# Optimization experiments

Hardware: AMD Instinct MI355X
Metric: run time of the kernel (lower is better)

## Reference

```python
import jax, jax.numpy as jnp
import numpy as np

HID, H, P, N, G, K = 2688, 64, 64, 128, 8, 4
I = H * P            # intermediate_size = 4096
GN = G * N           # groups_ssm_state_size = 1024
CONV_DIM = I + 2 * GN  # 6144
TOTAL = 2 * I + 2 * GN + H  # 10304
EPS = 1e-5


def setup_inputs() -> dict:
    key = jax.random.key(0)
    ks = jax.random.split(key, 8)
    B, T = 2, 2048
    hidden_states = jax.random.normal(ks[0], (B, T, HID), dtype=jnp.float32)
    in_proj_w = jax.random.normal(ks[1], (TOTAL, HID), dtype=jnp.float32) * 0.02
    conv_w = jax.random.normal(ks[2], (CONV_DIM, K), dtype=jnp.float32) * 0.1  # depthwise kernel
    conv_b = jnp.zeros((CONV_DIM,), dtype=jnp.float32)
    A = -jnp.exp(jax.random.normal(ks[3], (H,), dtype=jnp.float32))
    D = jnp.ones((H,), dtype=jnp.float32)
    dt_bias = jnp.ones((H,), dtype=jnp.float32)
    norm_weight = jnp.ones((I,), dtype=jnp.float32)
    out_proj_w = jax.random.normal(ks[4], (HID, I), dtype=jnp.float32) * 0.02
    return {"hidden_states": hidden_states, "in_proj_w": in_proj_w, "conv_w": conv_w,
            "conv_b": conv_b, "A": A, "D": D, "dt_bias": dt_bias,
            "norm_weight": norm_weight, "out_proj_w": out_proj_w}


def reference(hidden_states, in_proj_w, conv_w, conv_b, A, D, dt_bias, norm_weight, out_proj_w):
    B, T, _ = hidden_states.shape
    hpg = H // G  # heads per group

    # 1-2. in_proj and split
    proj = jnp.einsum('bth,oh->bto', hidden_states, in_proj_w)  # (B,T,TOTAL)
    gate = proj[..., :I]
    xBC = proj[..., I:I + CONV_DIM]
    dt = proj[..., I + CONV_DIM:]  # (B,T,H)

    # 3. causal depthwise conv1d (left-pad K-1, slice to T) + silu
    xp = jnp.pad(xBC, ((0, 0), (K - 1, 0), (0, 0)))
    conv = conv_b
    for i in range(K):  # tiny fixed kernel loop
        conv = conv + xp[:, i:i + T, :] * conv_w[:, i]
    conv = jax.nn.silu(conv)

    # 4-5. split and reshape
    x = conv[..., :I].reshape(B, T, H, P)
    Bm = conv[..., I:I + GN].reshape(B, T, G, N)
    Cm = conv[..., I + GN:].reshape(B, T, G, N)

    # 6. selective scan (precompute dt / A_bar outside the scan)
    dt_sp = jax.nn.softplus(dt + dt_bias)          # (B,T,H)
    A_bar = jnp.exp(A * dt_sp)                     # (B,T,H)
    xg = x.reshape(B, T, G, hpg, P)
    Ab = A_bar.reshape(B, T, G, hpg)
    dts = dt_sp.reshape(B, T, G, hpg)

    def step(h, inp):
        x_t, B_t, C_t, Ab_t, dt_t = inp  # (B,G,hpg,P),(B,G,N),(B,G,N),(B,G,hpg),(B,G,hpg)
        outer = dt_t[..., None, None] * x_t[..., None] * B_t[:, :, None, None, :]
        h = Ab_t[..., None, None] * h + outer      # (B,G,hpg,P,N)
        y_t = jnp.einsum('bghpn,bgn->bghp', h, C_t)
        return h, y_t

    inputs = (jnp.moveaxis(xg, 1, 0), jnp.moveaxis(Bm, 1, 0), jnp.moveaxis(Cm, 1, 0),
              jnp.moveaxis(Ab, 1, 0), jnp.moveaxis(dts, 1, 0))
    h0 = jnp.zeros((B, G, hpg, P, N), dtype=hidden_states.dtype)
    _, ys = jax.lax.scan(step, h0, inputs)         # (T,B,G,hpg,P)
    y = jnp.moveaxis(ys, 0, 1).reshape(B, T, H, P) + D[None, None, :, None] * x
    y = y.reshape(B, T, I)

    # 7. gated RMSNorm
    y = y * jax.nn.silu(gate)
    var = jnp.mean(y * y, axis=-1, keepdims=True)
    y = y * jax.lax.rsqrt(var + EPS) * norm_weight

    # 8. out_proj
    return jnp.einsum('bti,oi->bto', y, out_proj_w)
```

## Files before the change

### kernel.cpp

```cpp
#include <hip/hip_runtime.h>
#include <stdint.h>

typedef unsigned short ushort_t;
typedef __attribute__((ext_vector_type(4))) float f32x4;
typedef __attribute__((ext_vector_type(2))) float f32x2;
typedef __attribute__((ext_vector_type(8))) __bf16 bf16x8;
typedef __attribute__((ext_vector_type(4))) unsigned short u16x4;
typedef __attribute__((ext_vector_type(8))) unsigned short u16x8;

#define DEV __device__ __forceinline__

DEV void gload_lds16(const void* g, void* l) {
  __builtin_amdgcn_global_load_lds(
      (const __attribute__((address_space(1))) uint32_t*)(uintptr_t)(g),
      (__attribute__((address_space(3))) uint32_t*)(uintptr_t)(l), 16, 0, 0);
}

DEV ushort_t f2bf(float f) {
  union { float f; uint32_t u; } x; x.f = f;
  x.u += 0x7fffu + ((x.u >> 16) & 1u);
  return (ushort_t)(x.u >> 16);
}

DEV float bf2f(ushort_t u) {
  union { uint32_t u; float f; } x; x.u = (uint32_t)u << 16; return x.f;
}

DEV float siluf(float x) { return x / (1.f + expf(-x)); }

#define BAR asm volatile("s_barrier" ::: "memory")
#define LGKM0 do { asm volatile("s_waitcnt lgkmcnt(0)" ::: "memory"); \
                   __builtin_amdgcn_sched_barrier(0); } while (0)
#define VMCNT(n) asm volatile("s_waitcnt vmcnt(" #n ")" ::: "memory")

__global__ __launch_bounds__(256) void fill_kernel(float* p, float v, int n) {
  int i = blockIdx.x * 256 + threadIdx.x;
  if (i < n) p[i] = v;
}

__global__ __launch_bounds__(256) void cvt_bf16_kernel(const float* __restrict__ src,
                                                       ushort_t* __restrict__ dst,
                                                       int n_src4, int n_dst4) {
  int i = blockIdx.x * 256 + threadIdx.x;
  if (i >= n_dst4) return;
  f32x4 v;
  if (i < n_src4) v = *(const f32x4*)(src + (size_t)i * 4);
  else { v.x = 0.f; v.y = 0.f; v.z = 0.f; v.w = 0.f; }
  u16x4 o;
  o.x = f2bf(v.x); o.y = f2bf(v.y); o.z = f2bf(v.z); o.w = f2bf(v.w);
  *(u16x4*)(dst + (size_t)i * 4) = o;
}

DEV void ld_a4(const unsigned char* ab2, int mgofs, int ck0, int ck1, bf16x8 (&af)[4][2]) {
#pragma unroll
  for (int mi = 0; mi < 4; ++mi) {
    const unsigned char* p = ab2 + (mgofs + mi * 16) * 128;
    af[mi][0] = *(const bf16x8*)(p + ck0);
    af[mi][1] = *(const bf16x8*)(p + ck1);
  }
}

DEV void ld_b2(const unsigned char* bb2, int npofs, int ck0, int ck1, bf16x8 (&bf)[2][2]) {
#pragma unroll
  for (int ni = 0; ni < 2; ++ni) {
    const unsigned char* p = bb2 + (npofs + ni * 16) * 128;
    bf[ni][0] = *(const bf16x8*)(p + ck0);
    bf[ni][1] = *(const bf16x8*)(p + ck1);
  }
}

DEV void mm16(f32x4 (&acc)[8][4], const bf16x8 (&af)[4][2], const bf16x8 (&bf)[2][2],
              int mb, int nb) {
  __builtin_amdgcn_s_setprio(1);
#pragma unroll
  for (int mi = 0; mi < 4; ++mi)
#pragma unroll
    for (int ni = 0; ni < 2; ++ni)
#pragma unroll
      for (int kk = 0; kk < 2; ++kk)
        acc[mb + mi][nb + ni] = __builtin_amdgcn_mfma_f32_16x16x32_bf16(
            af[mi][kk], bf[ni][kk], acc[mb + mi][nb + ni], 0, 0, 0);
  __builtin_amdgcn_s_setprio(0);
}

DEV void stage2(const ushort_t* s0, const ushort_t* s1, unsigned char* d) {
  gload_lds16(s0, d);
  gload_lds16(s1, d + 8192);
}

template <int MODE>
__global__ __launch_bounds__(512, 1) void gemm8_kernel(const ushort_t* __restrict__ A,
                                                       const ushort_t* __restrict__ B,
                                                       void* __restrict__ C0,
                                                       void* __restrict__ C1,
                                                       int K, int NB, int NC, int niter) {
  __shared__ __align__(16) unsigned char lds[131072];
  const int tid = threadIdx.x;
  const int l = tid & 63, w = tid >> 6;
  const int wr = w >> 2, wc = w & 3;
  const int lr = l & 15, lk = l >> 4;
  const int xm = (lr & 7) << 4;
  const int ck0 = (lk * 16) ^ xm;
  const int ck1 = (64 + lk * 16) ^ xm;
  const int bm = blockIdx.x, bn = blockIdx.y;

  const int rr = (w << 3) + (l >> 3);
  const int cE = ((l & 7) ^ (l >> 3)) << 3;
  const int dstoff = w * 1024 + l * 16;

  const ushort_t* sA00 = A + (size_t)(bm * 256 +       rr) * K + cE;
  const ushort_t* sA01 = A + (size_t)(bm * 256 +  64 + rr) * K + cE;
  const ushort_t* sA10 = A + (size_t)(bm * 256 + 128 + rr) * K + cE;
  const ushort_t* sA11 = A + (size_t)(bm * 256 + 192 + rr) * K + cE;
  int rb0 = bn * 256 +       rr; if (rb0 > NB - 1) rb0 = NB - 1;
  int rb1 = bn * 256 +  64 + rr; if (rb1 > NB - 1) rb1 = NB - 1;
  int rb2 = bn * 256 + 128 + rr; if (rb2 > NB - 1) rb2 = NB - 1;
  int rb3 = bn * 256 + 192 + rr; if (rb3 > NB - 1) rb3 = NB - 1;
  const ushort_t* sB00 = B + (size_t)rb0 * K + cE;
  const ushort_t* sB01 = B + (size_t)rb1 * K + cE;
  const ushort_t* sB10 = B + (size_t)rb2 * K + cE;
  const ushort_t* sB11 = B + (size_t)rb3 * K + cE;

  const int aoff = wr * 16384 + lr * 128;
  const int boff = 32768 + (wc >> 1) * 16384 + ((wc & 1) * 64 + lr) * 128;

  f32x4 acc[8][4] = {};
  bf16x8 af[4][2], bf[2][2], bg[2][2];

  stage2(sA00, sA01, lds + dstoff);
  stage2(sA10, sA11, lds + 16384 + dstoff);
  stage2(sB00, sB01, lds + 32768 + dstoff);
  stage2(sB10, sB11, lds + 49152 + dstoff);
  stage2(sA00 + 64, sA01 + 64, lds + 65536 + dstoff);
  VMCNT(2);
  BAR;

  auto kpair = [&](int kt0, bool last) {
    const unsigned char* a0 = lds + aoff;
    const unsigned char* b0 = lds + boff;
    const unsigned char* a1 = lds + 65536 + aoff;
    const unsigned char* b1 = lds + 65536 + boff;
    const size_t c1 = (size_t)(kt0 + 1) * 64;
    const size_t c2 = (size_t)(kt0 + 2) * 64;
    const size_t c3 = (size_t)(kt0 + 3) * 64;
    ld_a4(a0, 0, ck0, ck1, af);
    ld_b2(b0, 0, ck0, ck1, bf);
    stage2(sA10 + c1, sA11 + c1, lds + 65536 + 16384 + dstoff);
    BAR; LGKM0; mm16(acc, af, bf, 0, 0); BAR;
    ld_b2(b0, 32, ck0, ck1, bg);
    stage2(sB00 + c1, sB01 + c1, lds + 65536 + 32768 + dstoff);
    BAR; LGKM0; mm16(acc, af, bg, 0, 2); BAR;
    ld_a4(a0, 64, ck0, ck1, af);
    stage2(sB10 + c1, sB11 + c1, lds + 65536 + 49152 + dstoff);
    BAR; LGKM0; mm16(acc, af, bg, 4, 2); BAR;
    ld_b2(b0, 0, ck0, ck1, bf);
    if (!last) { stage2(sA00 + c2, sA01 + c2, lds + dstoff); VMCNT(2); }
    else       { VMCNT(0); }
    BAR; LGKM0; mm16(acc, af, bf, 4, 0); BAR;
    ld_a4(a1, 0, ck0, ck1, af);
    ld_b2(b1, 0, ck0, ck1, bf);
    if (!last) stage2(sA10 + c2, sA11 + c2, lds + 16384 + dstoff);
    BAR; LGKM0; mm16(acc, af, bf, 0, 0); BAR;
    ld_b2(b1, 32, ck0, ck1, bg);
    if (!last) stage2(sB00 + c2, sB01 + c2, lds + 32768 + dstoff);
    BAR; LGKM0; mm16(acc, af, bg, 0, 2); BAR;
    ld_a4(a1, 64, ck0, ck1, af);
    if (!last) stage2(sB10 + c2, sB11 + c2, lds + 49152 + dstoff);
    BAR; LGKM0; mm16(acc, af, bg, 4, 2); BAR;
    ld_b2(b1, 0, ck0, ck1, bf);
    if (!last) { stage2(sA00 + c3, sA01 + c3, lds + 65536 + dstoff); VMCNT(2); }
    BAR; LGKM0; mm16(acc, af, bf, 4, 0); BAR;
  };

  for (int it = 0; it < niter - 1; ++it) kpair(2 * it, false);
  kpair(2 * (niter - 1), true);

  const int crow0 = bm * 256 + wr * 128 + (lk << 2);
  const int ccol0 = bn * 256 + wc * 64 + lr;
  if (MODE == 0) {
    ushort_t* gate = (ushort_t*)C0;
    ushort_t* xbc  = (ushort_t*)C1;
#pragma unroll
    for (int ni = 0; ni < 4; ++ni) {
      const int col = ccol0 + ni * 16;
      if (col < NC) {
        ushort_t* dst; size_t stride;
        if (col < 4096) { dst = gate + col; stride = 4096; }
        else            { dst = xbc + (col - 4096); stride = 6272; }
#pragma unroll
        for (int mi = 0; mi < 8; ++mi)
#pragma unroll
          for (int r = 0; r < 4; ++r)
            dst[(size_t)(crow0 + mi * 16 + r) * stride] = f2bf(acc[mi][ni][r]);
      }
    }
  } else {
    float* o = (float*)C0;
#pragma unroll
    for (int ni = 0; ni < 4; ++ni) {
      const int col = ccol0 + ni * 16;
      if (col < NC) {
#pragma unroll
        for (int mi = 0; mi < 8; ++mi)
#pragma unroll
          for (int r = 0; r < 4; ++r)
            o[(size_t)(crow0 + mi * 16 + r) * NC + col] = acc[mi][ni][r];
      }
    }
  }
}

__global__ __launch_bounds__(256) void conv_silu_kernel(const ushort_t* __restrict__ xbc,
                                                        const float* __restrict__ cw,
                                                        const float* __restrict__ cb,
                                                        ushort_t* __restrict__ out) {
  int idx = blockIdx.x * 256 + threadIdx.x;
  int c4 = (idx % 1536) << 2;
  int bt = idx / 1536;
  int t = bt & 2047;
  const ushort_t* base = xbc + (size_t)bt * 6272 + c4;
  f32x4 w0 = *(const f32x4*)&cw[(c4 + 0) * 4];
  f32x4 w1 = *(const f32x4*)&cw[(c4 + 1) * 4];
  f32x4 w2 = *(const f32x4*)&cw[(c4 + 2) * 4];
  f32x4 w3 = *(const f32x4*)&cw[(c4 + 3) * 4];
  f32x4 acc = *(const f32x4*)&cb[c4];
#pragma unroll
  for (int i = 0; i < 4; ++i) {
    int dt_ = i - 3;
    if (t + dt_ >= 0) {
      u16x4 xv = *(const u16x4*)(base + (ptrdiff_t)dt_ * 6272);
      acc.x += bf2f(xv.x) * w0[i];
      acc.y += bf2f(xv.y) * w1[i];
      acc.z += bf2f(xv.z) * w2[i];
      acc.w += bf2f(xv.w) * w3[i];
    }
  }
  u16x4 o;
  o.x = f2bf(siluf(acc.x)); o.y = f2bf(siluf(acc.y));
  o.z = f2bf(siluf(acc.z)); o.w = f2bf(siluf(acc.w));
  *(u16x4*)(out + (size_t)bt * 6144 + c4) = o;
}

__global__ __launch_bounds__(256) void dt_kernel(const ushort_t* __restrict__ xbc,
                                                 const float* __restrict__ dt_bias,
                                                 const float* __restrict__ Avec,
                                                 float* __restrict__ dtA) {
  int idx = blockIdx.x * 256 + threadIdx.x;
  int h = idx >> 12, bt = idx & 4095;
  float v = bf2f(xbc[(size_t)bt * 6272 + 6144 + h]) + dt_bias[h];
  float sp = fmaxf(v, 0.f) + log1pf(expf(-fabsf(v)));
  float ab = expf(Avec[h] * sp);
  dtA[(h << 13) + bt] = sp;
  dtA[(h << 13) + 4096 + bt] = ab;
}

__global__ __launch_bounds__(256) void scan_pass1_kernel(const ushort_t* __restrict__ conv,
                                                         const float* __restrict__ dtA,
                                                         const float* __restrict__ Dvec,
                                                         const float* __restrict__ Avec,
                                                         ushort_t* __restrict__ yssm,
                                                         ushort_t* __restrict__ hst,
                                                         float* __restrict__ abprod) {
  const int bid = blockIdx.x;
  const int ck = bid & 7;
  const int ph = (bid >> 3) & 1;
  const int h = (bid >> 4) & 63;
  const int b = bid >> 10;
  const int g = h >> 3;
  const int tid = threadIdx.x;
  const int lane = tid & 63;
  const int wave = tid >> 6;
  const int pg = tid & 15, ng = tid >> 4;
  const int p0 = pg << 1, n0 = ng << 3;

  __shared__ __align__(16) unsigned char sraw[2][4672];
  __shared__ __align__(16) float ypart[2][4][8][32];

  const int btbase = (b << 11) + (ck << 8);
  const float* dt0 = dtA + (h << 13) + btbase;
  const float* dt1 = dt0 + 4096;
  const float Dh = Dvec[h];
  const int xcol = (h << 6) + (ph << 5);
  const size_t hbase = (size_t)bid * 4096;

  auto stage = [&](int tb) {
    unsigned char* dst = sraw[tb & 1];
    const int t0 = tb << 3;
    const size_t row0 = (size_t)(btbase + t0) * 6144;
#pragma unroll
    for (int j = 0; j < 2; ++j) {
      int c = tid + (j << 8);
      if (c < 292) {
        const void* src;
        if (c < 32)       { src = conv + row0 + (size_t)(c >> 2) * 6144 + xcol + ((c & 3) << 3); }
        else if (c < 160) { int r = c - 32;  src = conv + row0 + (size_t)(r >> 4) * 6144 + 4096 + (g << 7) + ((r & 15) << 3); }
        else if (c < 288) { int r = c - 160; src = conv + row0 + (size_t)(r >> 4) * 6144 + 5120 + (g << 7) + ((r & 15) << 3); }
        else if (c < 290) { src = dt0 + t0 + ((c - 288) << 2); }
        else              { src = dt1 + t0 + ((c - 290) << 2); }
        gload_lds16(src, dst + ((size_t)c << 4));
      }
    }
  };

  stage(0);

  float hs0[8], hs1[8];
#pragma unroll
  for (int n = 0; n < 8; ++n) { hs0[n] = 0.f; hs1[n] = 0.f; }
  float dtsum = 0.f;

  for (int tb = 0; tb < 32; ++tb) {
    __syncthreads();
    if (tb > 0) {
      const int cur = (tb - 1) & 1;
      const int tprev = btbase + ((tb - 1) << 3);
      const int tt = tid >> 5, p = tid & 31;
      float v = ypart[cur][0][tt][p] + ypart[cur][1][tt][p] +
                ypart[cur][2][tt][p] + ypart[cur][3][tt][p];
      yssm[(size_t)(tprev + tt) * 4096 + xcol + p] = f2bf(v);
    }
    if (tb + 1 < 32) stage(tb + 1);
    const ushort_t* sbu = (const ushort_t*)sraw[tb & 1];
    const float* sfs = (const float*)(sraw[tb & 1] + 4608);
    const int cur = tb & 1;
#pragma unroll
    for (int tt = 0; tt < 8; ++tt) {
      uint32_t xv = *(const uint32_t*)&sbu[(tt << 5) + p0];
      float x0 = bf2f((ushort_t)xv), x1 = bf2f((ushort_t)(xv >> 16));
      u16x8 bv = *(const u16x8*)&sbu[256 + (tt << 7) + n0];
      u16x8 cv = *(const u16x8*)&sbu[1280 + (tt << 7) + n0];
      float dtv = sfs[tt], ab = sfs[8 + tt];
      dtsum += dtv;
      float dtx0 = dtv * x0, dtx1 = dtv * x1;
      float ys0 = 0.f, ys1 = 0.f;
#pragma unroll
      for (int n = 0; n < 8; ++n) {
        float Bn = bf2f(bv[n]), Cn = bf2f(cv[n]);
        hs0[n] = ab * hs0[n] + dtx0 * Bn; ys0 += hs0[n] * Cn;
        hs1[n] = ab * hs1[n] + dtx1 * Bn; ys1 += hs1[n] * Cn;
      }
      ys0 += __shfl_xor(ys0, 16, 64); ys0 += __shfl_xor(ys0, 32, 64);
      ys1 += __shfl_xor(ys1, 16, 64); ys1 += __shfl_xor(ys1, 32, 64);
      if (wave == 0) { ys0 += Dh * x0; ys1 += Dh * x1; }
      if ((lane >> 4) == 0) {
        f32x2 o; o.x = ys0; o.y = ys1;
        *(f32x2*)&ypart[cur][wave][tt][p0] = o;
      }
    }
  }
  {
    u16x8 o0, o1;
#pragma unroll
    for (int n = 0; n < 8; ++n) { o0[n] = f2bf(hs0[n]); o1[n] = f2bf(hs1[n]); }
    *(u16x8*)&hst[hbase + (size_t)p0 * 128 + n0] = o0;
    *(u16x8*)&hst[hbase + (size_t)(p0 + 1) * 128 + n0] = o1;
    if (ph == 0 && tid == 0)
      abprod[((b << 6) + h) * 8 + ck] = expf(Avec[h] * dtsum);
  }
  __syncthreads();
  {
    const int cur = 31 & 1;
    const int tprev = btbase + (31 << 3);
    const int tt = tid >> 5, p = tid & 31;
    float v = ypart[cur][0][tt][p] + ypart[cur][1][tt][p] +
              ypart[cur][2][tt][p] + ypart[cur][3][tt][p];
    yssm[(size_t)(tprev + tt) * 4096 + xcol + p] = f2bf(v);
  }
}

__global__ __launch_bounds__(256) void combine_kernel(ushort_t* __restrict__ hst,
                                                      const float* __restrict__ abprod) {
  const int bid = blockIdx.x;
  const int bh = bid >> 1;
  const int tid = threadIdx.x;
  const size_t base = (size_t)bid * 8 * 4096 + tid * 16;
  float hrun[16];
#pragma unroll
  for (int e = 0; e < 16; ++e) hrun[e] = 0.f;
  for (int c = 0; c < 8; ++c) {
    const size_t p = base + (size_t)c * 4096;
    u16x8 v0 = *(const u16x8*)&hst[p];
    u16x8 v1 = *(const u16x8*)&hst[p + 8];
    float ab = abprod[bh * 8 + c];
    u16x8 w0, w1;
#pragma unroll
    for (int e = 0; e < 8; ++e) { w0[e] = f2bf(hrun[e]); w1[e] = f2bf(hrun[8 + e]); }
    *(u16x8*)&hst[p] = w0;
    *(u16x8*)&hst[p + 8] = w1;
#pragma unroll
    for (int e = 0; e < 8; ++e) {
      hrun[e] = ab * hrun[e] + bf2f(v0[e]);
      hrun[8 + e] = ab * hrun[8 + e] + bf2f(v1[e]);
    }
  }
}

__global__ __launch_bounds__(256) void correct_kernel(const ushort_t* __restrict__ conv,
                                                      const float* __restrict__ dtA,
                                                      const float* __restrict__ Avec,
                                                      const ushort_t* __restrict__ hst,
                                                      ushort_t* __restrict__ yssm) {
  const int bid = blockIdx.x;
  const int ck = bid & 7;
  const int h = (bid >> 3) & 63;
  const int b = bid >> 9;
  const int g = h >> 3;
  const int tid = threadIdx.x;
  const int lane = tid & 63;
  const int w = tid >> 6;
  const int lr = lane & 15, lk = lane >> 4;
  const int btb = (b << 11) + (ck << 8);

  __shared__ float pdl[256];
  __shared__ float wsum[4];
  float s = dtA[(h << 13) + btb + tid];
#pragma unroll
  for (int off = 1; off < 64; off <<= 1) {
    float t = __shfl_up(s, off, 64);
    if (lane >= off) s += t;
  }
  if (lane == 63) wsum[w] = s;
  __syncthreads();
  float basev = 0.f;
  for (int i = 0; i < w; ++i) basev += wsum[i];
  pdl[tid] = expf(Avec[h] * (basev + s));
  __syncthreads();

  const ushort_t* Cc = conv + (size_t)btb * 6144 + 5120 + (g << 7);
  const size_t hb0 = ((size_t)((b << 10) | (h << 4) | (0 << 3) | ck)) * 4096;
  const size_t hb1 = ((size_t)((b << 10) | (h << 4) | (1 << 3) | ck)) * 4096;

  f32x4 acc[4][4] = {};
#pragma unroll
  for (int kk = 0; kk < 4; ++kk) {
    const int k0 = kk * 32 + lk * 8;
    bf16x8 afr[4], bfr[4];
#pragma unroll
    for (int mf = 0; mf < 4; ++mf) {
      const int t = w * 64 + mf * 16 + lr;
      afr[mf] = *(const bf16x8*)(Cc + (size_t)t * 6144 + k0);
    }
#pragma unroll
    for (int nf = 0; nf < 4; ++nf) {
      const int p = nf * 16 + lr;
      const size_t hb = (p < 32) ? hb0 : hb1;
      bfr[nf] = *(const bf16x8*)(hst + hb + (size_t)(p & 31) * 128 + k0);
    }
#pragma unroll
    for (int mf = 0; mf < 4; ++mf)
#pragma unroll
      for (int nf = 0; nf < 4; ++nf)
        acc[mf][nf] = __builtin_amdgcn_mfma_f32_16x16x32_bf16(afr[mf], bfr[nf],
                                                              acc[mf][nf], 0, 0, 0);
  }

#pragma unroll
  for (int mf = 0; mf < 4; ++mf) {
#pragma unroll
    for (int r = 0; r < 4; ++r) {
      const int row = w * 64 + mf * 16 + (lk << 2) + r;
      const float pd = pdl[row];
      const size_t yrow = (size_t)(btb + row) * 4096 + (h << 6);
#pragma unroll
      for (int nf = 0; nf < 4; ++nf) {
        const int p = nf * 16 + lr;
        const size_t idx = yrow + p;
        yssm[idx] = f2bf(bf2f(yssm[idx]) + pd * acc[mf][nf][r]);
      }
    }
  }
}

__global__ __launch_bounds__(256) void norm_kernel(const ushort_t* __restrict__ yssm,
                                                   const ushort_t* __restrict__ gate,
                                                   const float* __restrict__ nw,
                                                   ushort_t* __restrict__ out) {
  const int bt = blockIdx.x;
  const int tid = threadIdx.x;
  const ushort_t* y = yssm + (size_t)bt * 4096;
  const ushort_t* gt = gate + (size_t)bt * 4096;
  float vals[16];
  float ss = 0.f;
#pragma unroll
  for (int j = 0; j < 4; ++j) {
    int o = (tid + j * 256) << 2;
    u16x4 yv = *(const u16x4*)(y + o);
    u16x4 gv = *(const u16x4*)(gt + o);
#pragma unroll
    for (int e = 0; e < 4; ++e) {
      float v = bf2f(yv[e]) * siluf(bf2f(gv[e]));
      vals[j * 4 + e] = v;
      ss += v * v;
    }
  }
#pragma unroll
  for (int m = 1; m <= 32; m <<= 1) ss += __shfl_xor(ss, m, 64);
  __shared__ float red[4];
  if ((tid & 63) == 0) red[tid >> 6] = ss;
  __syncthreads();
  ss = red[0] + red[1] + red[2] + red[3];
  const float sc = rsqrtf(ss * (1.f / 4096.f) + 1e-5f);
#pragma unroll
  for (int j = 0; j < 4; ++j) {
    int o = (tid + j * 256) << 2;
    f32x4 wv = *(const f32x4*)(nw + o);
    u16x4 ov;
    ov.x = f2bf(vals[j * 4 + 0] * sc * wv.x);
    ov.y = f2bf(vals[j * 4 + 1] * sc * wv.y);
    ov.z = f2bf(vals[j * 4 + 2] * sc * wv.z);
    ov.w = f2bf(vals[j * 4 + 3] * sc * wv.w);
    *(u16x4*)(out + (size_t)bt * 4096 + o) = ov;
  }
}

extern "C" void kernel_launch(void* const* d_in, const int* in_sizes, int n_in,
                              void* d_out, int out_size, void* d_ws, size_t ws_size,
                              hipStream_t stream) {
  const float* hidden  = (const float*)d_in[0];
  const float* w_in    = (const float*)d_in[1];
  const float* conv_w  = (const float*)d_in[2];
  const float* conv_b  = (const float*)d_in[3];
  const float* Avec    = (const float*)d_in[4];
  const float* Dvec    = (const float*)d_in[5];
  const float* dt_bias = (const float*)d_in[6];
  const float* nw      = (const float*)d_in[7];
  const float* w_out   = (const float*)d_in[8];
  float* out = (float*)d_out;

  char* ws = (char*)d_ws;
  ushort_t* Xbf   = (ushort_t*)(ws);
  ushort_t* W1bf  = (ushort_t*)(ws + 22020096);
  ushort_t* gate  = (ushort_t*)(ws + 77758464);
  ushort_t* xbc   = (ushort_t*)(ws + 111312896);
  ushort_t* W2bf  = Xbf;
  ushort_t* convb = W1bf;
  float*    dtA   = (float*)(ws + 22020096 + 50331648);
  float*    abprod= (float*)(ws + 22020096 + 52428800);
  ushort_t* yssm  = xbc;
  ushort_t* hst   = (ushort_t*)(ws + 111312896 + 33554432);
  ushort_t* ynorm = convb;
  const size_t NEED = 162693120;
  if (NEED > ws_size) {
    fill_kernel<<<4, 256, 0, stream>>>(out, 12345.0f, 1024);
    return;
  }

  cvt_bf16_kernel<<<10752, 256, 0, stream>>>(hidden, Xbf, 2752512, 2752512);
  cvt_bf16_kernel<<<27216, 256, 0, stream>>>(w_in, W1bf, 6924288, 6967296);
  gemm8_kernel<0><<<dim3(16, 41), 512, 0, stream>>>(Xbf, W1bf, gate, xbc,
                                                    2688, 10368, 10304, 21);
  cvt_bf16_kernel<<<10752, 256, 0, stream>>>(w_out, W2bf, 2752512, 2752512);
  conv_silu_kernel<<<24576, 256, 0, stream>>>(xbc, conv_w, conv_b, convb);
  dt_kernel<<<1024, 256, 0, stream>>>(xbc, dt_bias, Avec, dtA);
  scan_pass1_kernel<<<2048, 256, 0, stream>>>(convb, dtA, Dvec, Avec, yssm, hst, abprod);
  combine_kernel<<<256, 256, 0, stream>>>(hst, abprod);
  correct_kernel<<<1024, 256, 0, stream>>>(convb, dtA, Avec, hst, yssm);
  norm_kernel<<<4096, 256, 0, stream>>>(yssm, gate, nw, ynorm);
  gemm8_kernel<1><<<dim3(16, 11), 512, 0, stream>>>(ynorm, W2bf, out, nullptr,
                                                    4096, 2688, 2688, 32);
}
```

Before: 789.9 us.

## Merge scan P-halves into one block and use packed f32x2 state math

The chunked-scan first pass now has each block cover all 64 P columns of a head instead of splitting them into two half-blocks. This halves the block count and avoids loading the shared B/C/dt tiles twice. Each thread keeps four state columns as packed f32x2 vectors, so the compiler can emit packed FMA instructions. The hst layout is preserved by computing the old half-block index, and the trade-off is more registers per thread and fewer blocks in flight.

```diff
diff --git a/kernel.cpp b/kernel.cpp
--- a/kernel.cpp
+++ b/kernel.cpp
@@ -263,25 +263,23 @@
                                                          float* __restrict__ abprod) {
   const int bid = blockIdx.x;
   const int ck = bid & 7;
-  const int ph = (bid >> 3) & 1;
-  const int h = (bid >> 4) & 63;
-  const int b = bid >> 10;
+  const int h = (bid >> 3) & 63;
+  const int b = bid >> 9;
   const int g = h >> 3;
   const int tid = threadIdx.x;
   const int lane = tid & 63;
   const int wave = tid >> 6;
   const int pg = tid & 15, ng = tid >> 4;
-  const int p0 = pg << 1, n0 = ng << 3;
-
-  __shared__ __align__(16) unsigned char sraw[2][4672];
-  __shared__ __align__(16) float ypart[2][4][8][32];
+  const int p0 = pg << 2, n0 = (ng & 15) << 3;
+
+  __shared__ __align__(16) unsigned char sraw[2][5184];
+  __shared__ __align__(16) float ypart[2][4][8][64];
 
   const int btbase = (b << 11) + (ck << 8);
   const float* dt0 = dtA + (h << 13) + btbase;
   const float* dt1 = dt0 + 4096;
   const float Dh = Dvec[h];
-  const int xcol = (h << 6) + (ph << 5);
-  const size_t hbase = (size_t)bid * 4096;
+  const int xcol = h << 6;
 
   auto stage = [&](int tb) {
     unsigned char* dst = sraw[tb & 1];
@@ -290,13 +288,13 @@
 #pragma unroll
     for (int j = 0; j < 2; ++j) {
       int c = tid + (j << 8);
-      if (c < 292) {
+      if (c < 324) {
         const void* src;
-        if (c < 32)       { src = conv + row0 + (size_t)(c >> 2) * 6144 + xcol + ((c & 3) << 3); }
-        else if (c < 160) { int r = c - 32;  src = conv + row0 + (size_t)(r >> 4) * 6144 + 4096 + (g << 7) + ((r & 15) << 3); }
-        else if (c < 288) { int r = c - 160; src = conv + row0 + (size_t)(r >> 4) * 6144 + 5120 + (g << 7) + ((r & 15) << 3); }
-        else if (c < 290) { src = dt0 + t0 + ((c - 288) << 2); }
-        else              { src = dt1 + t0 + ((c - 290) << 2); }
+        if (c < 64)       { src = conv + row0 + (size_t)(c >> 3) * 6144 + xcol + ((c & 7) << 3); }
+        else if (c < 192) { int r = c - 64;  src = conv + row0 + (size_t)(r >> 4) * 6144 + 4096 + (g << 7) + ((r & 15) << 3); }
+        else if (c < 320) { int r = c - 192; src = conv + row0 + (size_t)(r >> 4) * 6144 + 5120 + (g << 7) + ((r & 15) << 3); }
+        else if (c < 322) { src = dt0 + t0 + ((c - 320) << 2); }
+        else              { src = dt1 + t0 + ((c - 322) << 2); }
         gload_lds16(src, dst + ((size_t)c << 4));
       }
     }
@@ -304,9 +302,9 @@
 
   stage(0);
 
-  float hs0[8], hs1[8];
-#pragma unroll
-  for (int n = 0; n < 8; ++n) { hs0[n] = 0.f; hs1[n] = 0.f; }
+  f32x2 hsA[8], hsB[8];
+#pragma unroll
+  for (int n = 0; n < 8; ++n) { hsA[n] = (f32x2)(0.f); hsB[n] = (f32x2)(0.f); }
   float dtsum = 0.f;
 
   for (int tb = 0; tb < 32; ++tb) {
@@ -314,57 +312,86 @@
     if (tb > 0) {
       const int cur = (tb - 1) & 1;
       const int tprev = btbase + ((tb - 1) << 3);
-      const int tt = tid >> 5, p = tid & 31;
-      float v = ypart[cur][0][tt][p] + ypart[cur][1][tt][p] +
-                ypart[cur][2][tt][p] + ypart[cur][3][tt][p];
-      yssm[(size_t)(tprev + tt) * 4096 + xcol + p] = f2bf(v);
+#pragma unroll
+      for (int r2 = 0; r2 < 2; ++r2) {
+        int idx = tid + (r2 << 8);
+        int tt = idx >> 6, p = idx & 63;
+        float v = ypart[cur][0][tt][p] + ypart[cur][1][tt][p] +
+                  ypart[cur][2][tt][p] + ypart[cur][3][tt][p];
+        yssm[(size_t)(tprev + tt) * 4096 + xcol + p] = f2bf(v);
+      }
     }
     if (tb + 1 < 32) stage(tb + 1);
     const ushort_t* sbu = (const ushort_t*)sraw[tb & 1];
-    const float* sfs = (const float*)(sraw[tb & 1] + 4608);
+    const float* sfs = (const float*)(sraw[tb & 1] + 5120);
     const int cur = tb & 1;
 #pragma unroll
     for (int tt = 0; tt < 8; ++tt) {
-      uint32_t xv = *(const uint32_t*)&sbu[(tt << 5) + p0];
-      float x0 = bf2f((ushort_t)xv), x1 = bf2f((ushort_t)(xv >> 16));
-      u16x8 bv = *(const u16x8*)&sbu[256 + (tt << 7) + n0];
-      u16x8 cv = *(const u16x8*)&sbu[1280 + (tt << 7) + n0];
-      float dtv = sfs[tt], ab = sfs[8 + tt];
+      u16x4 xv = *(const u16x4*)&sbu[(tt << 6) + p0];
+      f32x2 xa, xb;
+      xa.x = bf2f(xv.x); xa.y = bf2f(xv.y);
+      xb.x = bf2f(xv.z); xb.y = bf2f(xv.w);
+      u16x8 bv = *(const u16x8*)&sbu[512 + (tt << 7) + n0];
+      u16x8 cv = *(const u16x8*)&sbu[1536 + (tt << 7) + n0];
+      const float dtv = sfs[tt], abv = sfs[8 + tt];
       dtsum += dtv;
-      float dtx0 = dtv * x0, dtx1 = dtv * x1;
-      float ys0 = 0.f, ys1 = 0.f;
+      f32x2 ab2; ab2.x = abv; ab2.y = abv;
+      f32x2 da = dtv * xa, db = dtv * xb;
+      f32x2 ya = (f32x2)(0.f), yb = (f32x2)(0.f);
 #pragma unroll
       for (int n = 0; n < 8; ++n) {
-        float Bn = bf2f(bv[n]), Cn = bf2f(cv[n]);
-        hs0[n] = ab * hs0[n] + dtx0 * Bn; ys0 += hs0[n] * Cn;
-        hs1[n] = ab * hs1[n] + dtx1 * Bn; ys1 += hs1[n] * Cn;
-      }
-      ys0 += __shfl_xor(ys0, 16, 64); ys0 += __shfl_xor(ys0, 32, 64);
-      ys1 += __shfl_xor(ys1, 16, 64); ys1 += __shfl_xor(ys1, 32, 64);
-      if (wave == 0) { ys0 += Dh * x0; ys1 += Dh * x1; }
+        const float Bn = bf2f(bv[n]);
+        const float Cn = bf2f(cv[n]);
+        f32x2 b2; b2.x = Bn; b2.y = Bn;
+        f32x2 c2; c2.x = Cn; c2.y = Cn;
+        hsA[n] = ab2 * hsA[n] + da * b2;  ya += hsA[n] * c2;
+        hsB[n] = ab2 * hsB[n] + db * b2;  yb += hsB[n] * c2;
+      }
+      float y0 = ya.x, y1 = ya.y, y2 = yb.x, y3 = yb.y;
+      y0 += __shfl_xor(y0, 16, 64); y0 += __shfl_xor(y0, 32, 64);
+      y1 += __shfl_xor(y1, 16, 64); y1 += __shfl_xor(y1, 32, 64);
+      y2 += __shfl_xor(y2, 16, 64); y2 += __shfl_xor(y2, 32, 64);
+      y3 += __shfl_xor(y3, 16, 64); y3 += __shfl_xor(y3, 32, 64);
+      if (wave == 0) {
+        y0 += Dh * xa.x; y1 += Dh * xa.y;
+        y2 += Dh * xb.x; y3 += Dh * xb.y;
+      }
       if ((lane >> 4) == 0) {
-        f32x2 o; o.x = ys0; o.y = ys1;
-        *(f32x2*)&ypart[cur][wave][tt][p0] = o;
+        f32x4 o; o.x = y0; o.y = y1; o.z = y2; o.w = y3;
+        *(f32x4*)&ypart[cur][wave][tt][p0] = o;
       }
     }
   }
   {
-    u16x8 o0, o1;
-#pragma unroll
-    for (int n = 0; n < 8; ++n) { o0[n] = f2bf(hs0[n]); o1[n] = f2bf(hs1[n]); }
-    *(u16x8*)&hst[hbase + (size_t)p0 * 128 + n0] = o0;
-    *(u16x8*)&hst[hbase + (size_t)(p0 + 1) * 128 + n0] = o1;
-    if (ph == 0 && tid == 0)
+#pragma unroll
+    for (int i = 0; i < 4; ++i) {
+      const int p = p0 + i;
+      const size_t hb = ((size_t)((b << 10) | (h << 4) | ((p >> 5) << 3) | ck)) * 4096;
+      u16x8 o;
+      if (i < 2) {
+#pragma unroll
+        for (int n = 0; n < 8; ++n) o[n] = f2bf((i == 0) ? hsA[n].x : hsA[n].y);
+      } else {
+#pragma unroll
+        for (int n = 0; n < 8; ++n) o[n] = f2bf((i == 2) ? hsB[n].x : hsB[n].y);
+      }
+      *(u16x8*)&hst[hb + (size_t)(p & 31) * 128 + n0] = o;
+    }
+    if (tid == 0)
       abprod[((b << 6) + h) * 8 + ck] = expf(Avec[h] * dtsum);
   }
   __syncthreads();
   {
     const int cur = 31 & 1;
     const int tprev = btbase + (31 << 3);
-    const int tt = tid >> 5, p = tid & 31;
-    float v = ypart[cur][0][tt][p] + ypart[cur][1][tt][p] +
-              ypart[cur][2][tt][p] + ypart[cur][3][tt][p];
-    yssm[(size_t)(tprev + tt) * 4096 + xcol + p] = f2bf(v);
+#pragma unroll
+    for (int r2 = 0; r2 < 2; ++r2) {
+      int idx = tid + (r2 << 8);
+      int tt = idx >> 6, p = idx & 63;
+      float v = ypart[cur][0][tt][p] + ypart[cur][1][tt][p] +
+                ypart[cur][2][tt][p] + ypart[cur][3][tt][p];
+      yssm[(size_t)(tprev + tt) * 4096 + xcol + p] = f2bf(v);
+    }
   }
 }
 
@@ -552,7 +579,7 @@
   cvt_bf16_kernel<<<10752, 256, 0, stream>>>(w_out, W2bf, 2752512, 2752512);
   conv_silu_kernel<<<24576, 256, 0, stream>>>(xbc, conv_w, conv_b, convb);
   dt_kernel<<<1024, 256, 0, stream>>>(xbc, dt_bias, Avec, dtA);
-  scan_pass1_kernel<<<2048, 256, 0, stream>>>(convb, dtA, Dvec, Avec, yssm, hst, abprod);
+  scan_pass1_kernel<<<1024, 256, 0, stream>>>(convb, dtA, Dvec, Avec, yssm, hst, abprod);
   combine_kernel<<<256, 256, 0, stream>>>(hst, abprod);
   correct_kernel<<<1024, 256, 0, stream>>>(convb, dtA, Avec, hst, yssm);
   norm_kernel<<<4096, 256, 0, stream>>>(yssm, gate, nw, ynorm);
```

New measurement: 727.8 us. 7.9% less time.

## Replace sequential chunk scan with SSD matmul formulation on MFMA

Applied to the files above, without the earlier changes.

Swaps the per-timestep recurrent scan inside each 256-step chunk for the Mamba2 SSD chunked form. The kernel builds a prefix sum of dt, computes the decayed chunk-end state as a bf16 MFMA matmul of X and weighted B, and computes intra-chunk outputs via a masked C·Bᵀ decay matrix times X, also on MFMA. This removes the serial dependency and the scalar FMA work, but adds bf16 rounding of intermediate products and heavy LDS use (about 75 KB per block), which lowers occupancy. It also drops two redundant B-fragment LDS reloads in the GEMM inner loop.

```diff
diff --git a/kernel.cpp b/kernel.cpp
--- a/kernel.cpp
+++ b/kernel.cpp
@@ -153,7 +153,6 @@
     ld_a4(a0, 64, ck0, ck1, af);
     stage2(sB10 + c1, sB11 + c1, lds + 65536 + 49152 + dstoff);
     BAR; LGKM0; mm16(acc, af, bg, 4, 2); BAR;
-    ld_b2(b0, 0, ck0, ck1, bf);
     if (!last) { stage2(sA00 + c2, sA01 + c2, lds + dstoff); VMCNT(2); }
     else       { VMCNT(0); }
     BAR; LGKM0; mm16(acc, af, bf, 4, 0); BAR;
@@ -167,7 +166,6 @@
     ld_a4(a1, 64, ck0, ck1, af);
     if (!last) stage2(sB10 + c2, sB11 + c2, lds + 49152 + dstoff);
     BAR; LGKM0; mm16(acc, af, bg, 4, 2); BAR;
-    ld_b2(b1, 0, ck0, ck1, bf);
     if (!last) { stage2(sA00 + c3, sA01 + c3, lds + 65536 + dstoff); VMCNT(2); }
     BAR; LGKM0; mm16(acc, af, bf, 4, 0); BAR;
   };
@@ -254,117 +252,180 @@
   dtA[(h << 13) + 4096 + bt] = ab;
 }
 
-__global__ __launch_bounds__(256) void scan_pass1_kernel(const ushort_t* __restrict__ conv,
-                                                         const float* __restrict__ dtA,
-                                                         const float* __restrict__ Dvec,
-                                                         const float* __restrict__ Avec,
-                                                         ushort_t* __restrict__ yssm,
-                                                         ushort_t* __restrict__ hst,
-                                                         float* __restrict__ abprod) {
+__global__ __launch_bounds__(256) void ssd_kernel(const ushort_t* __restrict__ conv,
+                                                  const float* __restrict__ dtA,
+                                                  const float* __restrict__ Dvec,
+                                                  const float* __restrict__ Avec,
+                                                  ushort_t* __restrict__ yssm,
+                                                  ushort_t* __restrict__ hst,
+                                                  float* __restrict__ abprod) {
   const int bid = blockIdx.x;
   const int ck = bid & 7;
-  const int ph = (bid >> 3) & 1;
-  const int h = (bid >> 4) & 63;
-  const int b = bid >> 10;
+  const int h = (bid >> 3) & 63;
+  const int b = bid >> 9;
   const int g = h >> 3;
   const int tid = threadIdx.x;
   const int lane = tid & 63;
-  const int wave = tid >> 6;
-  const int pg = tid & 15, ng = tid >> 4;
-  const int p0 = pg << 1, n0 = ng << 3;
-
-  __shared__ __align__(16) unsigned char sraw[2][4672];
-  __shared__ __align__(16) float ypart[2][4][8][32];
-
-  const int btbase = (b << 11) + (ck << 8);
-  const float* dt0 = dtA + (h << 13) + btbase;
-  const float* dt1 = dt0 + 4096;
+  const int wv = tid >> 6;
+  const int lr = lane & 15, lk = lane >> 4;
+  const int btb = (b << 11) + (ck << 8);
+
+  __shared__ __align__(16) unsigned char ldsb[76816];
+  float* csL = (float*)(ldsb + 73728);
+  float* dtL = (float*)(ldsb + 74752);
+  float* wL  = (float*)(ldsb + 75776);
+  float* wsum = (float*)(ldsb + 76800);
+
+  const float Ah = Avec[h];
   const float Dh = Dvec[h];
-  const int xcol = (h << 6) + (ph << 5);
-  const size_t hbase = (size_t)bid * 4096;
-
-  auto stage = [&](int tb) {
-    unsigned char* dst = sraw[tb & 1];
-    const int t0 = tb << 3;
-    const size_t row0 = (size_t)(btbase + t0) * 6144;
-#pragma unroll
-    for (int j = 0; j < 2; ++j) {
-      int c = tid + (j << 8);
-      if (c < 292) {
-        const void* src;
-        if (c < 32)       { src = conv + row0 + (size_t)(c >> 2) * 6144 + xcol + ((c & 3) << 3); }
-        else if (c < 160) { int r = c - 32;  src = conv + row0 + (size_t)(r >> 4) * 6144 + 4096 + (g << 7) + ((r & 15) << 3); }
-        else if (c < 288) { int r = c - 160; src = conv + row0 + (size_t)(r >> 4) * 6144 + 5120 + (g << 7) + ((r & 15) << 3); }
-        else if (c < 290) { src = dt0 + t0 + ((c - 288) << 2); }
-        else              { src = dt1 + t0 + ((c - 290) << 2); }
-        gload_lds16(src, dst + ((size_t)c << 4));
-      }
-    }
-  };
-
-  stage(0);
-
-  float hs0[8], hs1[8];
-#pragma unroll
-  for (int n = 0; n < 8; ++n) { hs0[n] = 0.f; hs1[n] = 0.f; }
-  float dtsum = 0.f;
-
-  for (int tb = 0; tb < 32; ++tb) {
+
+  float dv = dtA[(h << 13) + btb + tid];
+  float s = dv;
+#pragma unroll
+  for (int off = 1; off < 64; off <<= 1) {
+    float t = __shfl_up(s, off, 64);
+    if (lane >= off) s += t;
+  }
+  if (lane == 63) wsum[wv] = s;
+  __syncthreads();
+  float basev = 0.f;
+  for (int i = 0; i < wv; ++i) basev += wsum[i];
+  const float csv = basev + s;
+  csL[tid] = csv;
+  dtL[tid] = dv;
+  __syncthreads();
+  const float cstot = csL[255];
+  wL[tid] = dv * expf(Ah * (cstot - csv));
+  if (tid == 0) abprod[((b << 6) + h) * 8 + ck] = expf(Ah * cstot);
+
+  const ushort_t* Xg = conv + (size_t)btb * 6144 + (h << 6);
+#pragma unroll
+  for (int rep = 0; rep < 8; ++rep) {
+    int idx = rep * 256 + tid;
+    int t = idx >> 3, pq = (idx & 7) << 3;
+    u16x8 v = *(const u16x8*)(Xg + (size_t)t * 6144 + pq);
+#pragma unroll
+    for (int e = 0; e < 8; ++e) {
+      int p = pq + e;
+      *(ushort_t*)(ldsb + p * 512 + ((t * 2) ^ ((p & 7) << 4))) = v[e];
+    }
+  }
+  __syncthreads();
+
+  const ushort_t* Bg = conv + (size_t)btb * 6144 + 4096 + (g << 7);
+  f32x4 hacc[4][2] = {};
+  for (int tc = 0; tc < 8; ++tc) {
+#pragma unroll
+    for (int rep = 0; rep < 2; ++rep) {
+      int idx = rep * 256 + tid;
+      int tl = idx >> 4, nq = (idx & 15) << 3;
+      u16x8 v = *(const u16x8*)(Bg + (size_t)(tc * 32 + tl) * 6144 + nq);
+      float wt = wL[tc * 32 + tl];
+#pragma unroll
+      for (int e = 0; e < 8; ++e) {
+        int n = nq + e;
+        *(ushort_t*)(ldsb + 65536 + n * 64 + ((tl * 2) ^ ((n & 3) << 4))) =
+            f2bf(bf2f(v[e]) * wt);
+      }
+    }
     __syncthreads();
-    if (tb > 0) {
-      const int cur = (tb - 1) & 1;
-      const int tprev = btbase + ((tb - 1) << 3);
-      const int tt = tid >> 5, p = tid & 31;
-      float v = ypart[cur][0][tt][p] + ypart[cur][1][tt][p] +
-                ypart[cur][2][tt][p] + ypart[cur][3][tt][p];
-      yssm[(size_t)(tprev + tt) * 4096 + xcol + p] = f2bf(v);
-    }
-    if (tb + 1 < 32) stage(tb + 1);
-    const ushort_t* sbu = (const ushort_t*)sraw[tb & 1];
-    const float* sfs = (const float*)(sraw[tb & 1] + 4608);
-    const int cur = tb & 1;
-#pragma unroll
-    for (int tt = 0; tt < 8; ++tt) {
-      uint32_t xv = *(const uint32_t*)&sbu[(tt << 5) + p0];
-      float x0 = bf2f((ushort_t)xv), x1 = bf2f((ushort_t)(xv >> 16));
-      u16x8 bv = *(const u16x8*)&sbu[256 + (tt << 7) + n0];
-      u16x8 cv = *(const u16x8*)&sbu[1280 + (tt << 7) + n0];
-      float dtv = sfs[tt], ab = sfs[8 + tt];
-      dtsum += dtv;
-      float dtx0 = dtv * x0, dtx1 = dtv * x1;
-      float ys0 = 0.f, ys1 = 0.f;
-#pragma unroll
-      for (int n = 0; n < 8; ++n) {
-        float Bn = bf2f(bv[n]), Cn = bf2f(cv[n]);
-        hs0[n] = ab * hs0[n] + dtx0 * Bn; ys0 += hs0[n] * Cn;
-        hs1[n] = ab * hs1[n] + dtx1 * Bn; ys1 += hs1[n] * Cn;
-      }
-      ys0 += __shfl_xor(ys0, 16, 64); ys0 += __shfl_xor(ys0, 32, 64);
-      ys1 += __shfl_xor(ys1, 16, 64); ys1 += __shfl_xor(ys1, 32, 64);
-      if (wave == 0) { ys0 += Dh * x0; ys1 += Dh * x1; }
-      if ((lane >> 4) == 0) {
-        f32x2 o; o.x = ys0; o.y = ys1;
-        *(f32x2*)&ypart[cur][wave][tt][p0] = o;
-      }
-    }
-  }
-  {
-    u16x8 o0, o1;
-#pragma unroll
-    for (int n = 0; n < 8; ++n) { o0[n] = f2bf(hs0[n]); o1[n] = f2bf(hs1[n]); }
-    *(u16x8*)&hst[hbase + (size_t)p0 * 128 + n0] = o0;
-    *(u16x8*)&hst[hbase + (size_t)(p0 + 1) * 128 + n0] = o1;
-    if (ph == 0 && tid == 0)
-      abprod[((b << 6) + h) * 8 + ck] = expf(Avec[h] * dtsum);
-  }
-  __syncthreads();
-  {
-    const int cur = 31 & 1;
-    const int tprev = btbase + (31 << 3);
-    const int tt = tid >> 5, p = tid & 31;
-    float v = ypart[cur][0][tt][p] + ypart[cur][1][tt][p] +
-              ypart[cur][2][tt][p] + ypart[cur][3][tt][p];
-    yssm[(size_t)(tprev + tt) * 4096 + xcol + p] = f2bf(v);
+    bf16x8 a4[4], b2[2];
+#pragma unroll
+    for (int pf = 0; pf < 4; ++pf) {
+      int p = pf * 16 + lr;
+      a4[pf] = *(const bf16x8*)(ldsb + p * 512 + (((tc * 32 + lk * 8) * 2) ^ ((p & 7) << 4)));
+    }
+#pragma unroll
+    for (int nf = 0; nf < 2; ++nf) {
+      int n = wv * 32 + nf * 16 + lr;
+      b2[nf] = *(const bf16x8*)(ldsb + 65536 + n * 64 + ((lk * 16) ^ ((n & 3) << 4)));
+    }
+#pragma unroll
+    for (int pf = 0; pf < 4; ++pf)
+#pragma unroll
+      for (int nf = 0; nf < 2; ++nf)
+        hacc[pf][nf] = __builtin_amdgcn_mfma_f32_16x16x32_bf16(a4[pf], b2[nf],
+                                                               hacc[pf][nf], 0, 0, 0);
+    __syncthreads();
+  }
+#pragma unroll
+  for (int pf = 0; pf < 4; ++pf)
+#pragma unroll
+    for (int nf = 0; nf < 2; ++nf)
+#pragma unroll
+      for (int r = 0; r < 4; ++r) {
+        int p = pf * 16 + (lk << 2) + r;
+        int n = wv * 32 + nf * 16 + lr;
+        hst[((size_t)((b << 10) | (h << 4) | ((p >> 5) << 3) | ck)) * 4096 +
+            (size_t)(p & 31) * 128 + n] = f2bf(hacc[pf][nf][r]);
+      }
+
+  const ushort_t* Cg = conv + (size_t)btb * 6144 + 5120 + (g << 7);
+  for (int rb = 0; rb < 4; ++rb) {
+    const int i0 = rb << 6;
+    f32x4 sacc[4][4] = {};
+#pragma unroll
+    for (int kk = 0; kk < 4; ++kk) {
+      bf16x8 ca[4], bb[4];
+#pragma unroll
+      for (int ifr = 0; ifr < 4; ++ifr)
+        ca[ifr] = *(const bf16x8*)(Cg + (size_t)(i0 + ifr * 16 + lr) * 6144 + kk * 32 + lk * 8);
+#pragma unroll
+      for (int jf = 0; jf < 4; ++jf)
+        bb[jf] = *(const bf16x8*)(Bg + (size_t)(wv * 64 + jf * 16 + lr) * 6144 + kk * 32 + lk * 8);
+#pragma unroll
+      for (int ifr = 0; ifr < 4; ++ifr)
+#pragma unroll
+        for (int jf = 0; jf < 4; ++jf)
+          sacc[ifr][jf] = __builtin_amdgcn_mfma_f32_16x16x32_bf16(ca[ifr], bb[jf],
+                                                                  sacc[ifr][jf], 0, 0, 0);
+    }
+#pragma unroll
+    for (int ifr = 0; ifr < 4; ++ifr) {
+#pragma unroll
+      for (int jf = 0; jf < 4; ++jf) {
+        int j = wv * 64 + jf * 16 + lr;
+        float dtj = dtL[j], csj = csL[j];
+#pragma unroll
+        for (int r = 0; r < 4; ++r) {
+          int il = ifr * 16 + (lk << 2) + r;
+          int ig = i0 + il;
+          float val = 0.f;
+          if (j <= ig) val = sacc[ifr][jf][r] * dtj * expf(Ah * (csL[ig] - csj));
+          *(ushort_t*)(ldsb + 32768 + il * 512 + ((j * 2) ^ ((il & 7) << 4))) = f2bf(val);
+        }
+      }
+    }
+    __syncthreads();
+    f32x4 yacc[4] = {};
+    const int ilB = wv * 16 + lr;
+#pragma unroll
+    for (int ks = 0; ks < 8; ++ks) {
+      bf16x8 pb = *(const bf16x8*)(ldsb + 32768 + ilB * 512 +
+                                   (((ks * 32 + lk * 8) * 2) ^ ((ilB & 7) << 4)));
+#pragma unroll
+      for (int pf = 0; pf < 4; ++pf) {
+        int p = pf * 16 + lr;
+        bf16x8 pa = *(const bf16x8*)(ldsb + p * 512 +
+                                     (((ks * 32 + lk * 8) * 2) ^ ((p & 7) << 4)));
+        yacc[pf] = __builtin_amdgcn_mfma_f32_16x16x32_bf16(pa, pb, yacc[pf], 0, 0, 0);
+      }
+    }
+    const int irow = i0 + wv * 16 + lr;
+    const size_t ybase = (size_t)(btb + irow) * 4096 + (h << 6);
+#pragma unroll
+    for (int pf = 0; pf < 4; ++pf) {
+      u16x4 o;
+#pragma unroll
+      for (int r = 0; r < 4; ++r) {
+        int p = pf * 16 + (lk << 2) + r;
+        float xv = bf2f(*(const ushort_t*)(ldsb + p * 512 +
+                                           ((irow * 2) ^ ((p & 7) << 4))));
+        o[r] = f2bf(yacc[pf][r] + Dh * xv);
+      }
+      *(u16x4*)(yssm + ybase + pf * 16 + (lk << 2)) = o;
+    }
+    __syncthreads();
   }
 }
 
@@ -552,7 +613,7 @@
   cvt_bf16_kernel<<<10752, 256, 0, stream>>>(w_out, W2bf, 2752512, 2752512);
   conv_silu_kernel<<<24576, 256, 0, stream>>>(xbc, conv_w, conv_b, convb);
   dt_kernel<<<1024, 256, 0, stream>>>(xbc, dt_bias, Avec, dtA);
-  scan_pass1_kernel<<<2048, 256, 0, stream>>>(convb, dtA, Dvec, Avec, yssm, hst, abprod);
+  ssd_kernel<<<1024, 256, 0, stream>>>(convb, dtA, Dvec, Avec, yssm, hst, abprod);
   combine_kernel<<<256, 256, 0, stream>>>(hst, abprod);
   correct_kernel<<<1024, 256, 0, stream>>>(convb, dtA, Avec, hst, yssm);
   norm_kernel<<<4096, 256, 0, stream>>>(yssm, gate, nw, ynorm);
```

After: 748.9 us. 1.05x faster.
